# Kernel tuning notes

Measured on AMD Instinct MI355X. Metric: run time of the kernel, lower is better.

## Reference

```python
import jax, jax.numpy as jnp
import numpy as np
from functools import partial

# Config (BranchNet 'big'-style)
HIST = [42, 78, 150, 294, 582]
PW = [3, 6, 12, 24, 48]
SHIFTING = [False, False, True, True, True]
CW = 7          # conv width
F = 32          # conv filters
E = 32          # embedding dims
B = 4096        # batch
H_TOT = 590     # total history length
V = 8192        # 2**(pc_hash_bits+1)
WBITS = 2       # weight quantization bits
ABITS = 3       # activation quantization bits
EPS = 1e-5


@partial(jax.custom_vjp, nondiff_argnums=(1,))
def quant_signed(x, bits):
    # Quantize.forward (signed, bits>1): round(x*scale)/scale, scale=(1<<(bits-1))-1
    scale = float((1 << (bits - 1)) - 1)
    return jnp.round(x * scale) / scale

def _q_fwd(x, bits):
    return quant_signed(x, bits), None

def _q_bwd(bits, res, g):
    # straight-through estimator, matching Quantize.backward
    return (g,)

quant_signed.defvjp(_q_fwd, _q_bwd)


def batchnorm(x, gamma, beta, axes, pshape):
    # training-mode BatchNorm1d: batch statistics, biased variance
    m = jnp.mean(x, axis=axes, keepdims=True)
    v = jnp.var(x, axis=axes, keepdims=True)
    return gamma.reshape(pshape) * (x - m) * jax.lax.rsqrt(v + EPS) + beta.reshape(pshape)


def extract_slice_history(x, global_shift, slice_size, pooling_width, shifting):
    # vectorized version of the per-sample Python loop in extract_slice_history
    h_tot = x.shape[1]
    if shifting:
        s = jnp.mod(global_shift, pooling_width)              # [B]
        start = (h_tot - s - slice_size)[:, None]             # [B,1]
        idx = start + jnp.arange(slice_size)[None, :]         # [B,L]
        return jnp.take_along_axis(x, idx, axis=1)
    return x[:, -slice_size:]


def fc_layer(x, W, b, gamma, beta):
    # FCLayer with quantized weights + batchnorm + hardtanh + quantized act
    w = quant_signed(jnp.clip(W, -1.0, 1.0), WBITS)
    y = x @ w.T + b
    y = batchnorm(y, gamma, beta, (0,), (1, -1))
    y = jnp.clip(y, -1.0, 1.0)  # hardtanh
    return quant_signed(y, ABITS)


def branchnet_forward(x, global_shift, emb, conv_w, conv_b, bn1_g, bn1_b,
                      bnp_g, bnp_b, W1, b1, g1, be1, W2, b2, g2, be2, W3, b3):
    feats = []
    for i in range(len(HIST)):
        L, pw = HIST[i], PW[i]
        xs = extract_slice_history(x, global_shift, L, pw, SHIFTING[i])  # [B,L] int
        e = jnp.take(emb[i], xs, axis=0)                                 # [B,L,E]
        e = jnp.transpose(e, (0, 2, 1))                                  # [B,E,L]
        h = jax.lax.conv_general_dilated(
            e, conv_w[i], window_strides=(1,), padding='VALID',
            dimension_numbers=('NCH', 'OIH', 'NCH')) + conv_b[i][None, :, None]
        h = batchnorm(h, bn1_g[i], bn1_b[i], (0, 2), (1, -1, 1))
        h = jnp.tanh(h)
        T = (L - CW + 1) // pw                                           # = 12
        p = h[:, :, :T * pw].reshape(h.shape[0], F, T, pw).mean(axis=-1) # AvgPool1d
        p = batchnorm(p, bnp_g[i], bnp_b[i], (0, 2), (1, -1, 1))
        feats.append(p.reshape(p.shape[0], -1))                          # [B, F*T]
    z = jnp.concatenate(feats, axis=1)                                   # [B, 1920]
    z = fc_layer(z, W1, b1, g1, be1)
    z = fc_layer(z, W2, b2, g2, be2)
    w3 = quant_signed(jnp.clip(W3, -1.0, 1.0), WBITS)
    out = z @ w3.T + b3                                                  # [B,1]
    return out[:, 0]                                                     # squeeze(dim=1)


def setup_inputs() -> dict:
    key = jax.random.key(0)
    ks = jax.random.split(key, 12)
    return {
        'x': jax.random.randint(ks[0], (B, H_TOT), 0, V, dtype=jnp.int32),
        'global_shift': jax.random.randint(ks[1], (B,), 0, 48, dtype=jnp.int32),
        'emb': jax.random.normal(ks[2], (5, V, E), jnp.float32) * 0.1,
        'conv_w': jax.random.normal(ks[3], (5, F, E, CW), jnp.float32) * 0.1,
        'conv_b': jax.random.normal(ks[4], (5, F), jnp.float32) * 0.01,
        'bn1_g': jnp.ones((5, F), jnp.float32),
        'bn1_b': jnp.zeros((5, F), jnp.float32),
        'bnp_g': jnp.ones((5, F), jnp.float32),
        'bnp_b': jnp.zeros((5, F), jnp.float32),
        'W1': jax.random.uniform(ks[5], (2048, 1920), jnp.float32, -1.0, 1.0),
        'b1': jax.random.normal(ks[6], (2048,), jnp.float32) * 0.01,
        'g1': jnp.ones((2048,), jnp.float32),
        'be1': jnp.zeros((2048,), jnp.float32),
        'W2': jax.random.uniform(ks[7], (2048, 2048), jnp.float32, -1.0, 1.0),
        'b2': jax.random.normal(ks[8], (2048,), jnp.float32) * 0.01,
        'g2': jnp.ones((2048,), jnp.float32),
        'be2': jnp.zeros((2048,), jnp.float32),
        'W3': jax.random.uniform(ks[9], (1, 2048), jnp.float32, -1.0, 1.0),
        'b3': jax.random.normal(ks[10], (1,), jnp.float32) * 0.01,
    }


def reference(x, global_shift, emb, conv_w, conv_b, bn1_g, bn1_b, bnp_g, bnp_b,
              W1, b1, g1, be1, W2, b2, g2, be2, W3, b3):
    return branchnet_forward(x, global_shift, emb, conv_w, conv_b, bn1_g, bn1_b,
                             bnp_g, bnp_b, W1, b1, g1, be1, W2, b2, g2, be2, W3, b3)
```

## Files before the change

kernel.cpp:

```cpp
#include <hip/hip_runtime.h>
#include <cmath>

#define HTOT  590
#define BATCH 4096
#define VOCAB 8192

typedef _Float16 f16;
typedef __attribute__((ext_vector_type(8))) _Float16 f16x8;
typedef __attribute__((ext_vector_type(4))) _Float16 f16x4;
typedef __attribute__((ext_vector_type(4))) float f32x4;
typedef __attribute__((ext_vector_type(16))) float f32x16;

constexpr size_t OFF_EHL  = 0;
constexpr size_t OFF_WF   = 1310720;
constexpr size_t OFF_PA   = 1347584;
constexpr size_t OFF_PB   = 2921472;
constexpr size_t OFF_BN1  = 4494336;
constexpr size_t OFF_BNP  = 4494656;
constexpr size_t OFF_CP   = 4494976;
constexpr size_t OFF_BNF1 = 4626048;
constexpr size_t OFF_PRAW = 4630528;
constexpr size_t OFF_W1P  = 12494848;
constexpr size_t OFF_W2P  = 14460928;
constexpr size_t OFF_Y    = 16558080;
constexpr size_t OFF_BNF2 = 24946688;
constexpr size_t OFF_Z2K  = 0;
constexpr size_t OFF_Z3K  = 4194304;

__device__ __forceinline__ float qw(float w) {
  return rintf(fminf(fmaxf(w, -1.f), 1.f));
}
__device__ __forceinline__ float4 ld4(const float* p) {
  return *reinterpret_cast<const float4*>(p);
}
__device__ __forceinline__ float tanh_c(float u) {
  const float e = __expf(2.f*u);
  return 1.f - __fdividef(2.f, e + 1.f);
}

#define MF(A,B,C) __builtin_amdgcn_mfma_f32_32x32x16_f16(A,B,C,0,0,0)

__global__ __launch_bounds__(256) void k_eprep(const float* __restrict__ emb,
                                               f16* __restrict__ ehl)
{
  const int idx = blockIdx.x*256 + threadIdx.x;
  const int c = idx & 31, v = (idx >> 5) & 8191, slice = idx >> 18;
  const float val = emb[(size_t)(slice*VOCAB + v)*32 + c];
  const f16 hi = (f16)val;
  const f16 lo = (f16)((val - (float)hi)*2048.f);
  f16* row = ehl + (size_t)(slice*VOCAB + v)*64;
  row[c] = hi; row[32 + c] = lo;
}

__global__ __launch_bounds__(256) void k_wfprep(const float* __restrict__ convw,
                                                f16* __restrict__ wf)
{
  const int idx = blockIdx.x*256 + threadIdx.x;
  const int j = idx & 7, lane = (idx >> 3) & 63, hl = (idx >> 9) & 1, ks = (idx >> 10) & 1;
  const int kk = idx >> 11, k = kk % 7, slice = kk / 7;
  const int f = lane & 31, c = ks*16 + (lane >> 5)*8 + j;
  const float val = convw[((slice*32 + f)*32 + c)*7 + k];
  const f16 hi = (f16)val;
  wf[idx] = hl ? (f16)((val - (float)hi)*2048.f) : hi;
}

template<int PASS>
__global__ __launch_bounds__(256, 2) void k_convm(const int* __restrict__ x,
                                                  const int* __restrict__ gshift,
                                                  const float* __restrict__ ehl,
                                                  const float* __restrict__ wfrag,
                                                  const float* __restrict__ bn1,
                                                  float* __restrict__ z,
                                                  float* __restrict__ partials)
{
  const int b = blockIdx.x;
  const int type = blockIdx.y;
  const int tid = threadIdx.x;
  const int wid = tid >> 6, lane = tid & 63;
  const int lt = lane & 31, hf = lane >> 5;

  __shared__ float smem[9996];
  __shared__ int   tokid[294];
  __shared__ float stat[(PASS==0)?256:4];

  float* tokrow = smem;
  float* thbuf  = smem;
  float* poolb  = smem + 4224;

  const int gsv = gshift[b];
  const int NTOK = (type == 0) ? 270 : 294;

  for (int i = tid; i < NTOK; i += 256) {
    int xs, q = i;
    if (type == 0) {
      if (i < 42)       { xs = 548; }
      else if (i < 120) { xs = 512; q = i - 42; }
      else              { xs = 440 - gsv % 12; q = i - 120; }
    } else if (type == 1) xs = 296 - gsv % 24;
    else if (type == 2)   xs = 8 - gsv % 48;
    else                  xs = 8 - gsv % 48 + 288;
    int xi = xs + q; if (xi < 0) xi += HTOT;
    tokid[i] = x[b*HTOT + xi];
  }
  __syncthreads();

  for (int j = tid; j < NTOK*8; j += 256) {
    const int row = j >> 3, ch = j & 7;
    const int sl = (type == 0) ? (row < 42 ? 0 : (row < 120 ? 1 : 2)) : ((type == 1) ? 3 : 4);
    const float4 v = ld4(ehl + (size_t)(sl*VOCAB + tokid[row])*32 + ch*4);
    float* d = &tokrow[row*34 + ch*4];
    *reinterpret_cast<float2*>(d)     = make_float2(v.x, v.y);
    *reinterpret_cast<float2*>(d + 2) = make_float2(v.z, v.w);
  }
  __syncthreads();

  int slice, tb, nt, slotoff, ThV, pw, si;
  if (type == 0) {
    if      (wid == 0) { slice=0; tb=0;  nt=2; slotoff=0;   ThV=36;  pw=3;  si=0; }
    else if (wid == 1) { slice=1; tb=0;  nt=3; slotoff=42;  ThV=72;  pw=6;  si=1; }
    else if (wid == 2) { slice=2; tb=0;  nt=3; slotoff=120; ThV=144; pw=12; si=2; }
    else               { slice=2; tb=96; nt=2; slotoff=120; ThV=144; pw=12; si=2; }
  } else if (type == 1) {
    slice=3; pw=24; ThV=288; slotoff=0; si=0;
    tb = (wid == 0) ? 0 : 32 + wid*64; nt = (wid == 0) ? 3 : 2;
  } else if (type == 2) {
    slice=4; pw=48; ThV=288; slotoff=0; si=0;
    tb = (wid == 0) ? 0 : 32 + wid*64; nt = (wid == 0) ? 3 : 2;
  } else {
    slice=4; pw=48; ThV=576; slotoff=-288; si=0;
    tb = 288 + ((wid == 0) ? 0 : 32 + wid*64); nt = (wid == 0) ? 3 : 2;
  }
  const int wb = (type == 3) ? 6 : 0;

  const float* wfsl = wfrag + slice*7168;
  #define LDA(K,KS,HL) (*reinterpret_cast<const f16x8*>(wfsl + (((K)*2+(KS))*2+(HL))*256 + lane*4))

  f32x16 a0[3], a1[3];
  #pragma unroll
  for (int r = 0; r < 3; ++r) {
    #pragma unroll
    for (int i = 0; i < 16; ++i) { a0[r][i] = 0.f; a1[r][i] = 0.f; }
  }

  #pragma unroll 1
  for (int k = 0; k < 7; ++k) {
    const f16x8 wh0 = LDA(k,0,0), wl0 = LDA(k,0,1), wh1 = LDA(k,1,0), wl1 = LDA(k,1,1);
    #pragma unroll
    for (int r = 0; r < 3; ++r) if (r < nt) {
      const int slot = slotoff + tb + r*32 + lt + k;
      const float* rp = tokrow + slot*34 + hf*4;
      const f16x4 q0 = *(const f16x4*)(rp),      q1 = *(const f16x4*)(rp+2);
      const f16x4 q2 = *(const f16x4*)(rp+8),    q3 = *(const f16x4*)(rp+10);
      const f16x4 q4 = *(const f16x4*)(rp+16),   q5 = *(const f16x4*)(rp+18);
      const f16x4 q6 = *(const f16x4*)(rp+24),   q7 = *(const f16x4*)(rp+26);
      const f16x8 bh0 = __builtin_shufflevector(q0,q1,0,1,2,3,4,5,6,7);
      const f16x8 bh1 = __builtin_shufflevector(q2,q3,0,1,2,3,4,5,6,7);
      const f16x8 bl0 = __builtin_shufflevector(q4,q5,0,1,2,3,4,5,6,7);
      const f16x8 bl1 = __builtin_shufflevector(q6,q7,0,1,2,3,4,5,6,7);
      a0[r] = MF(wh0, bh0, a0[r]);
      a1[r] = MF(wh0, bl0, a1[r]);
      a1[r] = MF(wl0, bh0, a1[r]);
      a0[r] = MF(wh1, bh1, a0[r]);
      a1[r] = MF(wh1, bl1, a1[r]);
      a1[r] = MF(wl1, bh1, a1[r]);
    }
  }
  __syncthreads();

  if (PASS == 1) {
    for (int i = tid; i < 2304; i += 256) poolb[i] = 0.f;
  }
  __syncthreads();

  float sv1[16], sv2[16], A1v[16], B1v[16];
  if (PASS == 0) {
    #pragma unroll
    for (int i = 0; i < 16; ++i) { sv1[i] = 0.f; sv2[i] = 0.f; }
  } else {
    #pragma unroll
    for (int i = 0; i < 16; ++i) {
      const int fr = (i&3) + 8*(i>>2) + 4*hf;
      A1v[i] = bn1[slice*32 + fr];
      B1v[i] = bn1[160 + slice*32 + fr];
    }
  }

  #pragma unroll
  for (int r = 0; r < 3; ++r) if (r < nt) {
    const int tbg = tb + r*32;
    float h[16];
    #pragma unroll
    for (int i = 0; i < 16; ++i) h[i] = a0[r][i] + a1[r][i]*(1.f/2048.f);
    if (PASS == 0) {
      const bool tv = (tbg + lt) < ThV;
      #pragma unroll
      for (int i = 0; i < 16; ++i) {
        const float hv = tv ? h[i] : 0.f;
        sv1[i] += hv; sv2[i] += hv*hv;
      }
    } else {
      #pragma unroll
      for (int i = 0; i < 16; ++i) {
        const int fr = (i&3) + 8*(i>>2) + 4*hf;
        thbuf[wid*1056 + fr*33 + lt] = tanh_c(A1v[i]*h[i] + B1v[i]);
      }
      const int tvend = min(tbg + 32, ThV);
      const int wlo = tbg / pw, whi = (tvend - 1) / pw;
      for (int w = wlo; w <= whi; ++w) {
        const int lo = max(w*pw, tbg), hi2 = min((w+1)*pw, tvend);
        float s = 0.f;
        for (int t = lo + hf; t < hi2; t += 2) s += thbuf[wid*1056 + lt*33 + (t - tbg)];
        s += __shfl_xor(s, 32);
        if (hf == 0) {
          const int piece = (w*pw < tbg) ? 1 : 0;
          poolb[(si*12 + (w - wb))*64 + piece*32 + lt] = s;
        }
      }
    }
  }

  if (PASS == 0) {
    #pragma unroll
    for (int i = 0; i < 16; ++i) {
      #pragma unroll
      for (int m = 1; m < 32; m <<= 1) {
        sv1[i] += __shfl_xor(sv1[i], m, 32);
        sv2[i] += __shfl_xor(sv2[i], m, 32);
      }
    }
    if (lt == 0) {
      #pragma unroll
      for (int i = 0; i < 16; ++i) {
        stat[wid*64 + hf*32 + i*2]     = sv1[i];
        stat[wid*64 + hf*32 + i*2 + 1] = sv2[i];
      }
    }
  }
  __syncthreads();

  const int nch = (type == 0) ? 96 : 32;
  if (tid < nch) {
    const int sic = tid >> 5, f = tid & 31;
    const int sg = (type == 0) ? sic : ((type == 1) ? 3 : 4);
    const int P = (sg < 4) ? sg*32 + f : ((type == 2) ? 128 + f : 160 + f);
    float s1 = 0.f, s2 = 0.f;
    if (PASS == 0) {
      const int hfc = (f >> 2) & 1, ic = (f & 3) + 4*(f >> 3);
      #pragma unroll
      for (int w = 0; w < 4; ++w) {
        const int wsi = (type == 0) ? ((w < 2) ? w : 2) : 0;
        if (wsi == sic) {
          s1 += stat[w*64 + hfc*32 + ic*2];
          s2 += stat[w*64 + hfc*32 + ic*2 + 1];
        }
      }
    } else {
      const int pwc = (type == 0) ? ((sic == 0) ? 3 : (sic == 1) ? 6 : 12)
                                  : ((type == 1) ? 24 : 48);
      const int nwin = (type >= 2) ? 6 : 12;
      const int wbc = (type == 3) ? 6 : 0;
      const float inv = 1.f/(float)pwc;
      for (int wl = 0; wl < nwin; ++wl) {
        const float p = (poolb[(sic*12 + wl)*64 + f] + poolb[(sic*12 + wl)*64 + 32 + f]) * inv;
        z[(size_t)b*1920 + sg*384 + (wl + wbc)*32 + f] = p;
        s1 += p; s2 += p*p;
      }
    }
    partials[(size_t)b*384 + P*2]     = s1;
    partials[(size_t)b*384 + P*2 + 1] = s2;
  }
}

template<int PASS>
__global__ __launch_bounds__(256) void k_bnfinal(const float* __restrict__ partials,
                                                 const float* __restrict__ gamma,
                                                 const float* __restrict__ beta,
                                                 float* __restrict__ outAB)
{
  const int c = blockIdx.x;
  const int slice = c >> 5, f = c & 31;
  const int tid = threadIdx.x;
  double s1 = 0.0, s2 = 0.0;
  for (int b = tid; b < BATCH; b += 256) {
    const float* p = partials + (size_t)b*384;
    if (slice < 4) { s1 += p[(slice*32+f)*2]; s2 += p[(slice*32+f)*2+1]; }
    else {
      s1 += (double)p[(128+f)*2]   + (double)p[(160+f)*2];
      s2 += (double)p[(128+f)*2+1] + (double)p[(160+f)*2+1];
    }
  }
  __shared__ double r1[256], r2[256];
  r1[tid] = s1; r2[tid] = s2;
  __syncthreads();
  for (int off = 128; off > 0; off >>= 1) {
    if (tid < off) { r1[tid] += r1[tid+off]; r2[tid] += r2[tid+off]; }
    __syncthreads();
  }
  if (tid == 0) {
    long N;
    if (PASS == 0) { const long Tall[5] = {36,72,144,288,576}; N = (long)BATCH * Tall[slice]; }
    else           { N = (long)BATCH * 12; }
    const double m   = r1[0]/(double)N;
    const double var = r2[0]/(double)N - m*m;
    const float rstd = (float)(1.0/sqrt(var + 1e-5));
    const float Aa = gamma[c]*rstd;
    outAB[c]       = Aa;
    outAB[160 + c] = beta[c] - Aa*(float)m;
  }
}

__global__ __launch_bounds__(256) void k_znorm(float* __restrict__ zz,
                                               const float* __restrict__ bnp)
{
  const size_t i4 = (size_t)blockIdx.x*256 + threadIdx.x;
  const float4 v = ld4(zz + i4*4);
  const int j = (int)((i4*4) % 1920);
  const int slice = j / 384, f0 = j & 31;
  const float4 A = ld4(bnp + slice*32 + f0);
  const float4 B = ld4(bnp + 160 + slice*32 + f0);
  const float zn[4] = {v.x*A.x+B.x, v.y*A.y+B.y, v.z*A.z+B.z, v.w*A.w+B.w};
  uint4 pk;
  unsigned w[4];
  #pragma unroll
  for (int e = 0; e < 4; ++e) {
    const f16 hi = (f16)zn[e];
    const f16 lo = (f16)(zn[e] - (float)hi);
    w[e] = (unsigned)__builtin_bit_cast(unsigned short, hi)
         | ((unsigned)__builtin_bit_cast(unsigned short, lo) << 16);
  }
  pk.x = w[0]; pk.y = w[1]; pk.z = w[2]; pk.w = w[3];
  *reinterpret_cast<uint4*>(zz + i4*4) = pk;
}

__global__ __launch_bounds__(256) void k_wprep1(const float* __restrict__ W1,
                                                f16* __restrict__ W1p)
{
  const int idx = blockIdx.x*256 + threadIdx.x;
  const int n = idx / 1920, klds = idx - n*1920;
  const int slice = klds / 384, r = klds - slice*384;
  const int tp = r >> 5, f = r & 31;
  W1p[idx] = (f16)qw(W1[n*1920 + slice*384 + f*12 + tp]);
}

__global__ __launch_bounds__(256) void k_wprep2(const float* __restrict__ W2,
                                                f16* __restrict__ W2p)
{
  const size_t i4 = (size_t)blockIdx.x*256 + threadIdx.x;
  const float4 v = ld4(W2 + i4*4);
  f16x4 o;
  o[0] = (f16)qw(v.x); o[1] = (f16)qw(v.y); o[2] = (f16)qw(v.z); o[3] = (f16)qw(v.w);
  *reinterpret_cast<f16x4*>(&W2p[i4*4]) = o;
}

template<int SPLIT, int PACKED>
__global__ __launch_bounds__(256) void k_mfgemm(const f16* __restrict__ Ahi,
                                               const unsigned* __restrict__ Apk,
                                               const f16* __restrict__ Bp,
                                               float* __restrict__ C,
                                               const int K, const float oscale)
{
  __shared__ f16 sA[(SPLIT+1)*128][40];
  __shared__ f16 sB[128][40];
  const int tid = threadIdx.x;
  const int bm = blockIdx.y*128, bn = blockIdx.x*128;
  const int wid = tid >> 6, lane = tid & 63;
  const int wm = (wid >> 1)*64, wn = (wid & 1)*64;
  const int lgrp = lane >> 4, lrow = lane & 15;
  f32x4 acc[4][4];
  #pragma unroll
  for (int m = 0; m < 4; ++m)
    #pragma unroll
    for (int n = 0; n < 4; ++n) acc[m][n] = (f32x4){0.f,0.f,0.f,0.f};

  const int srow = tid >> 2, sc = (tid & 3)*8;
  for (int k0 = 0; k0 < K; k0 += 32) {
    #pragma unroll
    for (int u = 0; u < 2; ++u) {
      const int row = srow + u*64;
      if (PACKED) {
        const unsigned* ap = Apk + (size_t)(bm+row)*K + k0 + sc;
        const uint4 v0 = *reinterpret_cast<const uint4*>(ap);
        const uint4 v1 = *reinterpret_cast<const uint4*>(ap + 4);
        uint4 hi, lo;
        hi.x = (v0.x & 0xffffu) | (v0.y << 16);  hi.y = (v0.z & 0xffffu) | (v0.w << 16);
        hi.z = (v1.x & 0xffffu) | (v1.y << 16);  hi.w = (v1.z & 0xffffu) | (v1.w << 16);
        lo.x = (v0.x >> 16) | (v0.y & 0xffff0000u);  lo.y = (v0.z >> 16) | (v0.w & 0xffff0000u);
        lo.z = (v1.x >> 16) | (v1.y & 0xffff0000u);  lo.w = (v1.z >> 16) | (v1.w & 0xffff0000u);
        *reinterpret_cast<uint4*>(&sA[row][sc])     = hi;
        *reinterpret_cast<uint4*>(&sA[128+row][sc]) = lo;
      } else {
        const uint4 va = *reinterpret_cast<const uint4*>(&Ahi[(size_t)(bm+row)*K + k0 + sc]);
        *reinterpret_cast<uint4*>(&sA[row][sc]) = va;
      }
      const uint4 vb = *reinterpret_cast<const uint4*>(&Bp[(size_t)(bn+row)*K + k0 + sc]);
      *reinterpret_cast<uint4*>(&sB[row][sc]) = vb;
    }
    __syncthreads();
    f16x8 bf[4];
    #pragma unroll
    for (int n = 0; n < 4; ++n)
      bf[n] = *reinterpret_cast<const f16x8*>(&sB[wn + n*16 + lrow][lgrp*8]);
    #pragma unroll
    for (int m = 0; m < 4; ++m) {
      const f16x8 ah = *reinterpret_cast<const f16x8*>(&sA[wm + m*16 + lrow][lgrp*8]);
      #pragma unroll
      for (int n = 0; n < 4; ++n)
        acc[m][n] = __builtin_amdgcn_mfma_f32_16x16x32_f16(ah, bf[n], acc[m][n], 0, 0, 0);
      if (SPLIT) {
        const f16x8 al = *reinterpret_cast<const f16x8*>(&sA[128 + wm + m*16 + lrow][lgrp*8]);
        #pragma unroll
        for (int n = 0; n < 4; ++n)
          acc[m][n] = __builtin_amdgcn_mfma_f32_16x16x32_f16(al, bf[n], acc[m][n], 0, 0, 0);
      }
    }
    __syncthreads();
  }
  #pragma unroll
  for (int m = 0; m < 4; ++m)
    #pragma unroll
    for (int n = 0; n < 4; ++n) {
      const int col = bn + wn + n*16 + lrow;
      #pragma unroll
      for (int r = 0; r < 4; ++r)
        C[(size_t)(bm + wm + m*16 + lgrp*4 + r)*2048 + col] = acc[m][n][r]*oscale;
    }
}

__global__ __launch_bounds__(256) void k_colpart(const float* __restrict__ Y,
                                                 double* __restrict__ part, int N)
{
  const int c0 = blockIdx.x*64;
  const int chunk = blockIdx.y;
  const int tid = threadIdx.x;
  const int c = tid & 63, rq = tid >> 6;
  double s1 = 0.0, s2 = 0.0;
  const int rbase = chunk*256;
  for (int r = rbase + rq; r < rbase+256; r += 4) {
    const float v = Y[(size_t)r*N + c0 + c];
    s1 += (double)v; s2 += (double)v*(double)v;
  }
  __shared__ double r1[256], r2[256];
  r1[tid] = s1; r2[tid] = s2;
  __syncthreads();
  if (tid < 64) {
    const double a  = r1[tid]+r1[tid+64]+r1[tid+128]+r1[tid+192];
    const double cc = r2[tid]+r2[tid+64]+r2[tid+128]+r2[tid+192];
    part[(size_t)(c0+c)*32 + chunk*2]     = a;
    part[(size_t)(c0+c)*32 + chunk*2 + 1] = cc;
  }
}

__global__ __launch_bounds__(256) void k_colfinal(const double* __restrict__ part,
                                                  const float* __restrict__ gamma,
                                                  const float* __restrict__ beta,
                                                  float* __restrict__ bnfc, int N)
{
  const int c = blockIdx.x*256 + threadIdx.x;
  if (c >= N) return;
  double s1 = 0.0, s2 = 0.0;
  #pragma unroll
  for (int ch = 0; ch < 16; ++ch) {
    s1 += part[(size_t)c*32 + ch*2];
    s2 += part[(size_t)c*32 + ch*2 + 1];
  }
  const double m   = s1/4096.0;
  const double var = s2/4096.0 - m*m;
  const float rstd = (float)(1.0/sqrt(var + 1e-5));
  const float Aa = gamma[c]*rstd;
  bnfc[c]        = Aa;
  bnfc[2048 + c] = beta[c] - Aa*(float)m;
}

__global__ __launch_bounds__(256) void k_act(const float* __restrict__ Y,
                                             const float* __restrict__ bnfc,
                                             f16* __restrict__ Zk)
{
  const size_t i4 = (size_t)blockIdx.x*256 + threadIdx.x;
  const int cbase = (int)((i4*4) & 2047);
  const float4 v = ld4(Y + i4*4);
  const float4 A = ld4(bnfc + cbase);
  const float4 B = ld4(bnfc + 2048 + cbase);
  const float t[4] = {v.x*A.x+B.x, v.y*A.y+B.y, v.z*A.z+B.z, v.w*A.w+B.w};
  f16x4 o;
  #pragma unroll
  for (int e = 0; e < 4; ++e) {
    const float c = fminf(fmaxf(t[e], -1.f), 1.f);
    o[e] = (f16)rintf(c*3.f);
  }
  *reinterpret_cast<f16x4*>(&Zk[i4*4]) = o;
}

__global__ __launch_bounds__(256) void k_final(const f16* __restrict__ Z3,
                                               const float* __restrict__ W3,
                                               const float* __restrict__ b3,
                                               float* __restrict__ out)
{
  const int b = blockIdx.x;
  const int tid = threadIdx.x;
  float s = 0.f;
  for (int j = tid; j < 2048; j += 256)
    s += (float)Z3[(size_t)b*2048 + j] * qw(W3[j]);
  __shared__ float red[256];
  red[tid] = s;
  __syncthreads();
  for (int off = 128; off > 0; off >>= 1) {
    if (tid < off) red[tid] += red[tid+off];
    __syncthreads();
  }
  if (tid == 0) out[b] = red[0]*(1.f/3.f) + b3[0];
}

extern "C" void kernel_launch(void* const* d_in, const int* in_sizes, int n_in,
                              void* d_out, int out_size, void* d_ws, size_t ws_size,
                              hipStream_t stream)
{
  const int*   x    = (const int*)d_in[0];
  const int*   gs   = (const int*)d_in[1];
  const float* emb  = (const float*)d_in[2];
  const float* cw   = (const float*)d_in[3];
  const float* bn1g = (const float*)d_in[5];
  const float* bn1b = (const float*)d_in[6];
  const float* bnpg = (const float*)d_in[7];
  const float* bnpb = (const float*)d_in[8];
  const float* W1   = (const float*)d_in[9];
  const float* g1   = (const float*)d_in[11];
  const float* be1  = (const float*)d_in[12];
  const float* W2   = (const float*)d_in[13];
  const float* g2   = (const float*)d_in[15];
  const float* be2  = (const float*)d_in[16];
  const float* W3   = (const float*)d_in[17];
  const float* b3   = (const float*)d_in[18];
  float* ws  = (float*)d_ws;
  float* out = (float*)d_out;

  k_eprep<<<5120, 256, 0, stream>>>(emb, (f16*)(ws + OFF_EHL));
  k_wfprep<<<280, 256, 0, stream>>>(cw, (f16*)(ws + OFF_WF));

  k_convm<0><<<dim3(BATCH, 4), 256, 0, stream>>>(x, gs, ws + OFF_EHL, ws + OFF_WF,
                                                 ws + OFF_BN1, nullptr, ws + OFF_PA);
  k_bnfinal<0><<<160, 256, 0, stream>>>(ws + OFF_PA, bn1g, bn1b, ws + OFF_BN1);
  k_convm<1><<<dim3(BATCH, 4), 256, 0, stream>>>(x, gs, ws + OFF_EHL, ws + OFF_WF,
                                                 ws + OFF_BN1, ws + OFF_PRAW, ws + OFF_PB);
  k_bnfinal<1><<<160, 256, 0, stream>>>(ws + OFF_PB, bnpg, bnpb, ws + OFF_BNP);
  k_znorm<<<7680, 256, 0, stream>>>(ws + OFF_PRAW, ws + OFF_BNP);
  k_wprep1<<<15360, 256, 0, stream>>>(W1, (f16*)(ws + OFF_W1P));
  k_wprep2<<<4096, 256, 0, stream>>>(W2, (f16*)(ws + OFF_W2P));

  k_mfgemm<1,1><<<dim3(16, 32), 256, 0, stream>>>(nullptr, (const unsigned*)(ws + OFF_PRAW),
                                                  (const f16*)(ws + OFF_W1P),
                                                  ws + OFF_Y, 1920, 1.f);
  k_colpart<<<dim3(32, 16), 256, 0, stream>>>(ws + OFF_Y, (double*)(ws + OFF_CP), 2048);
  k_colfinal<<<8, 256, 0, stream>>>((const double*)(ws + OFF_CP), g1, be1, ws + OFF_BNF1, 2048);
  k_act<<<8192, 256, 0, stream>>>(ws + OFF_Y, ws + OFF_BNF1, (f16*)(ws + OFF_Z2K));

  k_mfgemm<0,0><<<dim3(16, 32), 256, 0, stream>>>((const f16*)(ws + OFF_Z2K), nullptr,
                                                  (const f16*)(ws + OFF_W2P),
                                                  ws + OFF_Y, 2048, 1.f/3.f);
  k_colpart<<<dim3(32, 16), 256, 0, stream>>>(ws + OFF_Y, (double*)(ws + OFF_CP), 2048);
  k_colfinal<<<8, 256, 0, stream>>>((const double*)(ws + OFF_CP), g2, be2, ws + OFF_BNF2, 2048);
  k_act<<<8192, 256, 0, stream>>>(ws + OFF_Y, ws + OFF_BNF2, (f16*)(ws + OFF_Z3K));

  k_final<<<4096, 256, 0, stream>>>((const f16*)(ws + OFF_Z3K), W3, b3, out);
}
```

Before: 908.1 us.

## Cache conv outputs in global memory between stat and pooling passes

Pass 0 now writes each conv output as a packed fp16 hi/lo pair into a large workspace buffer. Pass 1 reads these back instead of redoing the embedding gather and the MFMA convolution. The token row stride in LDS changes from 34 to 36 floats, so B operands load as aligned f16x8 without shuffles, and the k loop is fully unrolled. Batch statistics are now reduced through an LDS fp16 staging buffer instead of warp shuffles, and occupancy is raised to 3 blocks per CU. The cache is about 600 MB of global write plus read traffic and is used only when the workspace is large enough. Rounding the statistics input to fp16 slightly changes numerics.

Result: faster. 834.4 us (-8.1%).

```diff
diff --git a/kernel.cpp b/kernel.cpp
--- a/kernel.cpp
+++ b/kernel.cpp
@@ -26,6 +26,8 @@
 constexpr size_t OFF_BNF2 = 24946688;
 constexpr size_t OFF_Z2K  = 0;
 constexpr size_t OFF_Z3K  = 4194304;
+constexpr size_t OFF_H    = 24950784;
+constexpr size_t END_H    = 180140032;
 
 __device__ __forceinline__ float qw(float w) {
   return rintf(fminf(fmaxf(w, -1.f), 1.f));
@@ -64,14 +66,15 @@
   wf[idx] = hl ? (f16)((val - (float)hi)*2048.f) : hi;
 }
 
-template<int PASS>
-__global__ __launch_bounds__(256, 2) void k_convm(const int* __restrict__ x,
+template<int PASS, int H>
+__global__ __launch_bounds__(256, 3) void k_convm(const int* __restrict__ x,
                                                   const int* __restrict__ gshift,
                                                   const float* __restrict__ ehl,
                                                   const float* __restrict__ wfrag,
                                                   const float* __restrict__ bn1,
                                                   float* __restrict__ z,
-                                                  float* __restrict__ partials)
+                                                  float* __restrict__ partials,
+                                                  unsigned* __restrict__ hbuf)
 {
   const int b = blockIdx.x;
   const int type = blockIdx.y;
@@ -79,40 +82,40 @@
   const int wid = tid >> 6, lane = tid & 63;
   const int lt = lane & 31, hf = lane >> 5;
 
-  __shared__ float smem[9996];
+  __shared__ float smem[10584];
   __shared__ int   tokid[294];
-  __shared__ float stat[(PASS==0)?256:4];
 
   float* tokrow = smem;
   float* thbuf  = smem;
   float* poolb  = smem + 4224;
+  f16*   hstat  = (f16*)smem;
+  float* part2  = smem + 6000;
 
   const int gsv = gshift[b];
   const int NTOK = (type == 0) ? 270 : 294;
 
-  for (int i = tid; i < NTOK; i += 256) {
-    int xs, q = i;
-    if (type == 0) {
-      if (i < 42)       { xs = 548; }
-      else if (i < 120) { xs = 512; q = i - 42; }
-      else              { xs = 440 - gsv % 12; q = i - 120; }
-    } else if (type == 1) xs = 296 - gsv % 24;
-    else if (type == 2)   xs = 8 - gsv % 48;
-    else                  xs = 8 - gsv % 48 + 288;
-    int xi = xs + q; if (xi < 0) xi += HTOT;
-    tokid[i] = x[b*HTOT + xi];
-  }
-  __syncthreads();
-
-  for (int j = tid; j < NTOK*8; j += 256) {
-    const int row = j >> 3, ch = j & 7;
-    const int sl = (type == 0) ? (row < 42 ? 0 : (row < 120 ? 1 : 2)) : ((type == 1) ? 3 : 4);
-    const float4 v = ld4(ehl + (size_t)(sl*VOCAB + tokid[row])*32 + ch*4);
-    float* d = &tokrow[row*34 + ch*4];
-    *reinterpret_cast<float2*>(d)     = make_float2(v.x, v.y);
-    *reinterpret_cast<float2*>(d + 2) = make_float2(v.z, v.w);
-  }
-  __syncthreads();
+  if (!(PASS == 1 && H == 1)) {
+    for (int i = tid; i < NTOK; i += 256) {
+      int xs, q = i;
+      if (type == 0) {
+        if (i < 42)       { xs = 548; }
+        else if (i < 120) { xs = 512; q = i - 42; }
+        else              { xs = 440 - gsv % 12; q = i - 120; }
+      } else if (type == 1) xs = 296 - gsv % 24;
+      else if (type == 2)   xs = 8 - gsv % 48;
+      else                  xs = 8 - gsv % 48 + 288;
+      int xi = xs + q; if (xi < 0) xi += HTOT;
+      tokid[i] = x[b*HTOT + xi];
+    }
+    __syncthreads();
+    for (int j = tid; j < NTOK*8; j += 256) {
+      const int row = j >> 3, ch = j & 7;
+      const int sl = (type == 0) ? (row < 42 ? 0 : (row < 120 ? 1 : 2)) : ((type == 1) ? 3 : 4);
+      const float4 v = ld4(ehl + (size_t)(sl*VOCAB + tokid[row])*32 + ch*4);
+      *reinterpret_cast<float4*>(&tokrow[row*36 + ch*4]) = v;
+    }
+    __syncthreads();
+  }
 
   int slice, tb, nt, slotoff, ThV, pw, si;
   if (type == 0) {
@@ -131,108 +134,128 @@
     tb = 288 + ((wid == 0) ? 0 : 32 + wid*64); nt = (wid == 0) ? 3 : 2;
   }
   const int wb = (type == 3) ? 6 : 0;
+  const int slot0 = (type == 0) ? ((wid == 0) ? 0 : (wid == 1) ? 2 : (wid == 2) ? 5 : 8)
+                                : ((wid == 0) ? 0 : 1 + wid*2);
+  const int tbase = (type == 0) ? 0 : 10 + (type - 1)*9;
 
   const float* wfsl = wfrag + slice*7168;
   #define LDA(K,KS,HL) (*reinterpret_cast<const f16x8*>(wfsl + (((K)*2+(KS))*2+(HL))*256 + lane*4))
 
   f32x16 a0[3], a1[3];
-  #pragma unroll
-  for (int r = 0; r < 3; ++r) {
-    #pragma unroll
-    for (int i = 0; i < 16; ++i) { a0[r][i] = 0.f; a1[r][i] = 0.f; }
-  }
-
-  #pragma unroll 1
-  for (int k = 0; k < 7; ++k) {
-    const f16x8 wh0 = LDA(k,0,0), wl0 = LDA(k,0,1), wh1 = LDA(k,1,0), wl1 = LDA(k,1,1);
+
+  if (!(PASS == 1 && H == 1)) {
+    #pragma unroll
+    for (int r = 0; r < 3; ++r) {
+      #pragma unroll
+      for (int i = 0; i < 16; ++i) { a0[r][i] = 0.f; a1[r][i] = 0.f; }
+    }
+    const float* pb = tokrow + (size_t)(slotoff + tb + lt)*36 + hf*4;
+    #pragma unroll
+    for (int k = 0; k < 7; ++k) {
+      const f16x8 wh0 = LDA(k,0,0), wl0 = LDA(k,0,1), wh1 = LDA(k,1,0), wl1 = LDA(k,1,1);
+      #pragma unroll
+      for (int r = 0; r < 3; ++r) if (r < nt) {
+        const float* rp = pb + k*36 + r*1152;
+        const f16x8 bh0 = *(const f16x8*)(rp),    bh1 = *(const f16x8*)(rp+8);
+        const f16x8 bl0 = *(const f16x8*)(rp+16), bl1 = *(const f16x8*)(rp+24);
+        a0[r]=MF(wh0,bh0,a0[r]); a1[r]=MF(wh0,bl0,a1[r]); a1[r]=MF(wl0,bh0,a1[r]);
+        a0[r]=MF(wh1,bh1,a0[r]); a1[r]=MF(wh1,bl1,a1[r]); a1[r]=MF(wl1,bh1,a1[r]);
+      }
+    }
+    __syncthreads();
+  }
+
+  if (PASS == 0) {
     #pragma unroll
     for (int r = 0; r < 3; ++r) if (r < nt) {
-      const int slot = slotoff + tb + r*32 + lt + k;
-      const float* rp = tokrow + slot*34 + hf*4;
-      const f16x4 q0 = *(const f16x4*)(rp),      q1 = *(const f16x4*)(rp+2);
-      const f16x4 q2 = *(const f16x4*)(rp+8),    q3 = *(const f16x4*)(rp+10);
-      const f16x4 q4 = *(const f16x4*)(rp+16),   q5 = *(const f16x4*)(rp+18);
-      const f16x4 q6 = *(const f16x4*)(rp+24),   q7 = *(const f16x4*)(rp+26);
-      const f16x8 bh0 = __builtin_shufflevector(q0,q1,0,1,2,3,4,5,6,7);
-      const f16x8 bh1 = __builtin_shufflevector(q2,q3,0,1,2,3,4,5,6,7);
-      const f16x8 bl0 = __builtin_shufflevector(q4,q5,0,1,2,3,4,5,6,7);
-      const f16x8 bl1 = __builtin_shufflevector(q6,q7,0,1,2,3,4,5,6,7);
-      a0[r] = MF(wh0, bh0, a0[r]);
-      a1[r] = MF(wh0, bl0, a1[r]);
-      a1[r] = MF(wl0, bh0, a1[r]);
-      a0[r] = MF(wh1, bh1, a0[r]);
-      a1[r] = MF(wh1, bl1, a1[r]);
-      a1[r] = MF(wl1, bh1, a1[r]);
-    }
-  }
-  __syncthreads();
-
-  if (PASS == 1) {
-    for (int i = tid; i < 2304; i += 256) poolb[i] = 0.f;
-  }
-  __syncthreads();
-
-  float sv1[16], sv2[16], A1v[16], B1v[16];
-  if (PASS == 0) {
-    #pragma unroll
-    for (int i = 0; i < 16; ++i) { sv1[i] = 0.f; sv2[i] = 0.f; }
-  } else {
-    #pragma unroll
-    for (int i = 0; i < 16; ++i) {
-      const int fr = (i&3) + 8*(i>>2) + 4*hf;
-      A1v[i] = bn1[slice*32 + fr];
-      B1v[i] = bn1[160 + slice*32 + fr];
-    }
-  }
-
-  #pragma unroll
-  for (int r = 0; r < 3; ++r) if (r < nt) {
-    const int tbg = tb + r*32;
-    float h[16];
-    #pragma unroll
-    for (int i = 0; i < 16; ++i) h[i] = a0[r][i] + a1[r][i]*(1.f/2048.f);
-    if (PASS == 0) {
-      const bool tv = (tbg + lt) < ThV;
-      #pragma unroll
-      for (int i = 0; i < 16; ++i) {
-        const float hv = tv ? h[i] : 0.f;
-        sv1[i] += hv; sv2[i] += hv*hv;
-      }
-    } else {
+      const int tbg = tb + r*32;
+      const int slot = slot0 + r;
+      unsigned* hd = H ? (hbuf + ((size_t)b*37 + tbase + slot)*1024 + lt) : nullptr;
       #pragma unroll
       for (int i = 0; i < 16; ++i) {
         const int fr = (i&3) + 8*(i>>2) + 4*hf;
-        thbuf[wid*1056 + fr*33 + lt] = tanh_c(A1v[i]*h[i] + B1v[i]);
-      }
-      const int tvend = min(tbg + 32, ThV);
-      const int wlo = tbg / pw, whi = (tvend - 1) / pw;
-      for (int w = wlo; w <= whi; ++w) {
-        const int lo = max(w*pw, tbg), hi2 = min((w+1)*pw, tvend);
-        float s = 0.f;
-        for (int t = lo + hf; t < hi2; t += 2) s += thbuf[wid*1056 + lt*33 + (t - tbg)];
-        s += __shfl_xor(s, 32);
-        if (hf == 0) {
-          const int piece = (w*pw < tbg) ? 1 : 0;
-          poolb[(si*12 + (w - wb))*64 + piece*32 + lt] = s;
+        const float h = a0[r][i] + a1[r][i]*(1.f/2048.f);
+        if (H) {
+          const f16 hi = (f16)h;
+          const f16 lo = (f16)((h - (float)hi)*2048.f);
+          hd[fr*32] = (unsigned)__builtin_bit_cast(unsigned short, hi)
+                    | ((unsigned)__builtin_bit_cast(unsigned short, lo) << 16);
         }
-      }
-    }
-  }
-
-  if (PASS == 0) {
+        const float hv = (tbg + lt < ThV) ? h : 0.f;
+        hstat[slot*1088 + fr*34 + lt] = (f16)hv;
+      }
+    }
+    __syncthreads();
+    const int nslot = (type == 0) ? 10 : 9;
+    for (int j = tid; j < nslot*32; j += 256) {
+      const int slot = j >> 5, f = j & 31;
+      const f16* rowp = hstat + slot*1088 + f*34;
+      float s1 = 0.f, s2 = 0.f;
+      #pragma unroll
+      for (int t = 0; t < 32; ++t) { const float v = (float)rowp[t]; s1 += v; s2 += v*v; }
+      part2[(slot*32 + f)*2]     = s1;
+      part2[(slot*32 + f)*2 + 1] = s2;
+    }
+    __syncthreads();
+    const int nch = (type == 0) ? 96 : 32;
+    if (tid < nch) {
+      const int sic = tid >> 5, f = tid & 31;
+      int slo, shi, Pb;
+      if (type == 0) {
+        slo = (sic == 0) ? 0 : (sic == 1) ? 2 : 5;
+        shi = (sic == 0) ? 2 : (sic == 1) ? 5 : 10;
+        Pb  = sic*32;
+      } else { slo = 0; shi = 9; Pb = 96 + (type - 1)*32; }
+      float s1 = 0.f, s2 = 0.f;
+      for (int s = slo; s < shi; ++s) {
+        s1 += part2[(s*32 + f)*2];
+        s2 += part2[(s*32 + f)*2 + 1];
+      }
+      partials[(size_t)b*384 + (Pb + f)*2]     = s1;
+      partials[(size_t)b*384 + (Pb + f)*2 + 1] = s2;
+    }
+    return;
+  }
+
+  for (int i = tid; i < 2304; i += 256) poolb[i] = 0.f;
+  __syncthreads();
+
+  float A1v[16], B1v[16];
+  #pragma unroll
+  for (int i = 0; i < 16; ++i) {
+    const int fr = (i&3) + 8*(i>>2) + 4*hf;
+    A1v[i] = bn1[slice*32 + fr];
+    B1v[i] = bn1[160 + slice*32 + fr];
+  }
+
+  #pragma unroll
+  for (int r = 0; r < 3; ++r) if (r < nt) {
+    const int tbg = tb + r*32;
+    const unsigned* hs = H ? (hbuf + ((size_t)b*37 + tbase + slot0 + r)*1024 + lt) : nullptr;
     #pragma unroll
     for (int i = 0; i < 16; ++i) {
-      #pragma unroll
-      for (int m = 1; m < 32; m <<= 1) {
-        sv1[i] += __shfl_xor(sv1[i], m, 32);
-        sv2[i] += __shfl_xor(sv2[i], m, 32);
-      }
-    }
-    if (lt == 0) {
-      #pragma unroll
-      for (int i = 0; i < 16; ++i) {
-        stat[wid*64 + hf*32 + i*2]     = sv1[i];
-        stat[wid*64 + hf*32 + i*2 + 1] = sv2[i];
+      const int fr = (i&3) + 8*(i>>2) + 4*hf;
+      float h;
+      if (H) {
+        const unsigned w = hs[fr*32];
+        const f16 hi = __builtin_bit_cast(f16, (unsigned short)(w & 0xffffu));
+        const f16 lo = __builtin_bit_cast(f16, (unsigned short)(w >> 16));
+        h = (float)hi + (float)lo*(1.f/2048.f);
+      } else {
+        h = a0[r][i] + a1[r][i]*(1.f/2048.f);
+      }
+      thbuf[wid*1056 + fr*33 + lt] = tanh_c(A1v[i]*h + B1v[i]);
+    }
+    const int tvend = min(tbg + 32, ThV);
+    const int wlo = tbg / pw, whi = (tvend - 1) / pw;
+    for (int w = wlo; w <= whi; ++w) {
+      const int lo = max(w*pw, tbg), hi2 = min((w+1)*pw, tvend);
+      float s = 0.f;
+      for (int t = lo + hf; t < hi2; t += 2) s += thbuf[wid*1056 + lt*33 + (t - tbg)];
+      s += __shfl_xor(s, 32);
+      if (hf == 0) {
+        const int piece = (w*pw < tbg) ? 1 : 0;
+        poolb[(si*12 + (w - wb))*64 + piece*32 + lt] = s;
       }
     }
   }
@@ -243,28 +266,16 @@
     const int sic = tid >> 5, f = tid & 31;
     const int sg = (type == 0) ? sic : ((type == 1) ? 3 : 4);
     const int P = (sg < 4) ? sg*32 + f : ((type == 2) ? 128 + f : 160 + f);
+    const int pwc = (type == 0) ? ((sic == 0) ? 3 : (sic == 1) ? 6 : 12)
+                                : ((type == 1) ? 24 : 48);
+    const int nwin = (type >= 2) ? 6 : 12;
+    const int wbc = (type == 3) ? 6 : 0;
+    const float inv = 1.f/(float)pwc;
     float s1 = 0.f, s2 = 0.f;
-    if (PASS == 0) {
-      const int hfc = (f >> 2) & 1, ic = (f & 3) + 4*(f >> 3);
-      #pragma unroll
-      for (int w = 0; w < 4; ++w) {
-        const int wsi = (type == 0) ? ((w < 2) ? w : 2) : 0;
-        if (wsi == sic) {
-          s1 += stat[w*64 + hfc*32 + ic*2];
-          s2 += stat[w*64 + hfc*32 + ic*2 + 1];
-        }
-      }
-    } else {
-      const int pwc = (type == 0) ? ((sic == 0) ? 3 : (sic == 1) ? 6 : 12)
-                                  : ((type == 1) ? 24 : 48);
-      const int nwin = (type >= 2) ? 6 : 12;
-      const int wbc = (type == 3) ? 6 : 0;
-      const float inv = 1.f/(float)pwc;
-      for (int wl = 0; wl < nwin; ++wl) {
-        const float p = (poolb[(sic*12 + wl)*64 + f] + poolb[(sic*12 + wl)*64 + 32 + f]) * inv;
-        z[(size_t)b*1920 + sg*384 + (wl + wbc)*32 + f] = p;
-        s1 += p; s2 += p*p;
-      }
+    for (int wl = 0; wl < nwin; ++wl) {
+      const float p = (poolb[(sic*12 + wl)*64 + f] + poolb[(sic*12 + wl)*64 + 32 + f]) * inv;
+      z[(size_t)b*1920 + sg*384 + (wl + wbc)*32 + f] = p;
+      s1 += p; s2 += p*p;
     }
     partials[(size_t)b*384 + P*2]     = s1;
     partials[(size_t)b*384 + P*2 + 1] = s2;
@@ -533,14 +544,25 @@
   float* ws  = (float*)d_ws;
   float* out = (float*)d_out;
 
+  const bool useH = ws_size >= (size_t)END_H * 4ull;
+  unsigned* hbuf = (unsigned*)(ws + OFF_H);
+
   k_eprep<<<5120, 256, 0, stream>>>(emb, (f16*)(ws + OFF_EHL));
   k_wfprep<<<280, 256, 0, stream>>>(cw, (f16*)(ws + OFF_WF));
 
-  k_convm<0><<<dim3(BATCH, 4), 256, 0, stream>>>(x, gs, ws + OFF_EHL, ws + OFF_WF,
-                                                 ws + OFF_BN1, nullptr, ws + OFF_PA);
-  k_bnfinal<0><<<160, 256, 0, stream>>>(ws + OFF_PA, bn1g, bn1b, ws + OFF_BN1);
-  k_convm<1><<<dim3(BATCH, 4), 256, 0, stream>>>(x, gs, ws + OFF_EHL, ws + OFF_WF,
-                                                 ws + OFF_BN1, ws + OFF_PRAW, ws + OFF_PB);
+  if (useH) {
+    k_convm<0,1><<<dim3(BATCH, 4), 256, 0, stream>>>(x, gs, ws + OFF_EHL, ws + OFF_WF,
+                                                     ws + OFF_BN1, nullptr, ws + OFF_PA, hbuf);
+    k_bnfinal<0><<<160, 256, 0, stream>>>(ws + OFF_PA, bn1g, bn1b, ws + OFF_BN1);
+    k_convm<1,1><<<dim3(BATCH, 4), 256, 0, stream>>>(x, gs, ws + OFF_EHL, ws + OFF_WF,
+                                                     ws + OFF_BN1, ws + OFF_PRAW, ws + OFF_PB, hbuf);
+  } else {
+    k_convm<0,0><<<dim3(BATCH, 4), 256, 0, stream>>>(x, gs, ws + OFF_EHL, ws + OFF_WF,
+                                                     ws + OFF_BN1, nullptr, ws + OFF_PA, hbuf);
+    k_bnfinal<0><<<160, 256, 0, stream>>>(ws + OFF_PA, bn1g, bn1b, ws + OFF_BN1);
+    k_convm<1,0><<<dim3(BATCH, 4), 256, 0, stream>>>(x, gs, ws + OFF_EHL, ws + OFF_WF,
+                                                     ws + OFF_BN1, ws + OFF_PRAW, ws + OFF_PB, hbuf);
+  }
   k_bnfinal<1><<<160, 256, 0, stream>>>(ws + OFF_PB, bnpg, bnpb, ws + OFF_BNP);
   k_znorm<<<7680, 256, 0, stream>>>(ws + OFF_PRAW, ws + OFF_BNP);
   k_wprep1<<<15360, 256, 0, stream>>>(W1, (f16*)(ws + OFF_W1P));
```
